# Kernel optimization log

Measured on AMD Instinct MI355X. Metric: run time of the kernel, lower is better.

The kernel has to match this reference:

```python
import jax, jax.numpy as jnp
import numpy as np

NUM_GRAPHS = 64  # number of graphs in the batch (static for segment reductions)


def gcn_conv(x, row, col, ew, W, b, N):
    """PyG GCNConv: x@W, symmetric gcn_norm with self-loops (weight 1), scatter-add, +bias."""
    xw = x @ W  # [N, F_out]
    # degree includes self-loop weight of 1.0 per node
    deg = jnp.zeros((N,), x.dtype).at[col].add(ew) + 1.0
    dis = jnp.where(deg > 0, jax.lax.rsqrt(deg), 0.0)  # deg^{-1/2}, inf -> 0
    norm = dis[row] * ew * dis[col]  # [E]
    agg = jnp.zeros_like(xw).at[col].add(xw[row] * norm[:, None])
    agg = agg + xw * (dis * dis)[:, None]  # self-loop contribution: 1/deg
    return agg + b


def global_mean_pool(x, batch, num_graphs):
    s = jnp.zeros((num_graphs, x.shape[1]), x.dtype).at[batch].add(x)
    cnt = jnp.zeros((num_graphs,), x.dtype).at[batch].add(1.0)
    return s / jnp.maximum(cnt, 1.0)[:, None]


def setup_inputs() -> dict:
    key = jax.random.key(0)
    ks = jax.random.split(key, 10)
    N, E, C_in, C_hid, C_out = 40000, 640000, 128, 128, 64
    flat = 6 * 22 * 22  # num_time_intervals * (2*num_nodes)^2 = 2904
    x = jax.random.normal(ks[0], (N, C_in), jnp.float32)
    edge_index = jax.random.randint(ks[1], (2, E), 0, N, jnp.int64)
    edge_weight = jax.random.uniform(ks[2], (E,), jnp.float32)
    batch = jnp.sort(jax.random.randint(ks[3], (N,), 0, NUM_GRAPHS, jnp.int64))
    W1 = jax.random.normal(ks[4], (C_in, C_hid), jnp.float32) / np.sqrt(C_in)
    b1 = jnp.zeros((C_hid,), jnp.float32)
    W2 = jax.random.normal(ks[5], (C_hid, C_out), jnp.float32) / np.sqrt(C_hid)
    b2 = jnp.zeros((C_out,), jnp.float32)
    Wfc = jax.random.normal(ks[6], (C_out, flat), jnp.float32) / np.sqrt(C_out)
    bfc = jnp.zeros((flat,), jnp.float32)
    return {"x": x, "edge_index": edge_index, "edge_weight": edge_weight, "batch": batch,
            "W1": W1, "b1": b1, "W2": W2, "b2": b2, "Wfc": Wfc, "bfc": bfc}


def reference(x, edge_index, edge_weight, batch, W1, b1, W2, b2, Wfc, bfc):
    N = x.shape[0]
    row, col = edge_index[0], edge_index[1]
    h = jax.nn.relu(gcn_conv(x, row, col, edge_weight, W1, b1, N))
    h = jax.nn.relu(gcn_conv(h, row, col, edge_weight, W2, b2, N))
    g = global_mean_pool(h, batch, NUM_GRAPHS)  # [G, C_out]
    return g @ Wfc + bfc  # [G, 2904] predicted flattened adjacency
```

## Files before the change

### kernel.cpp

```cpp
#include <hip/hip_runtime.h>
#include <hip/hip_bf16.h>
#include <hip/hip_fp16.h>
#include <type_traits>

#define NG 64
#define FLAT 2904
#define K128 128
#define BKB 256

typedef _Float16 h4 __attribute__((ext_vector_type(4)));
typedef _Float16 half8 __attribute__((ext_vector_type(8)));
typedef float f32x4 __attribute__((ext_vector_type(4)));

__device__ __forceinline__ float4 ld4(const float* p) { return *(const float4*)p; }
__device__ __forceinline__ void st4(float* p, float4 v) { *(float4*)p = v; }
__device__ __forceinline__ float4 ldh4(const _Float16* p) {
    h4 h = *(const h4*)p;
    return make_float4((float)h.x, (float)h.y, (float)h.z, (float)h.w);
}
__device__ __forceinline__ void sth4(_Float16* p, float4 v) {
    h4 h; h.x = (_Float16)v.x; h.y = (_Float16)v.y; h.z = (_Float16)v.z; h.w = (_Float16)v.w;
    *(h4*)p = h;
}

__global__ __launch_bounds__(256) void k_zero(int* __restrict__ bhist,
                                              float* __restrict__ g,
                                              int* __restrict__ gcnt) {
    int tid = threadIdx.x;
    for (int i = tid; i < BKB; i += 256) bhist[i] = 0;
    for (int i = tid; i < NG * 64; i += 256) g[i] = 0.f;
    if (tid < NG) gcnt[tid] = 0;
}


__global__ __launch_bounds__(256) void k_bhist(const int* __restrict__ col,
                                               int* __restrict__ bhist, int E, int nbk) {
    __shared__ int h[BKB];
    int tid = threadIdx.x;
    for (int i = tid; i < nbk; i += 256) h[i] = 0;
    __syncthreads();
    int base = blockIdx.x * 1024 + tid * 4;
#pragma unroll
    for (int q = 0; q < 4; q++) {
        int e = base + q;
        if (e < E) atomicAdd(&h[col[e] >> 8], 1);
    }
    __syncthreads();
    for (int i = tid; i < nbk; i += 256) if (h[i]) atomicAdd(&bhist[i], h[i]);
}

__global__ __launch_bounds__(256) void k_bscan(const int* __restrict__ bhist,
                                               int* __restrict__ bbase,
                                               int* __restrict__ bcursor,
                                               int* __restrict__ rsN, int E, int nbk) {
    __shared__ int part[256];
    int tid = threadIdx.x;
    int v = (tid < nbk) ? bhist[tid] : 0;
    part[tid] = v;
    __syncthreads();
    for (int off = 1; off < 256; off <<= 1) {
        int t = (tid >= off) ? part[tid - off] : 0;
        __syncthreads();
        part[tid] += t;
        __syncthreads();
    }
    if (tid < nbk) { int ex = part[tid] - v; bbase[tid] = ex; bcursor[tid] = ex; }
    if (tid == nbk - 1) bbase[nbk] = part[tid];
    if (tid == 0) *rsN = E;
}

__global__ __launch_bounds__(256) void k_bucket(const int* __restrict__ row,
                                                const int* __restrict__ col,
                                                const float* __restrict__ ew,
                                                int* __restrict__ bcursor,
                                                uint2* __restrict__ bk, int E, int nbk) {
    __shared__ int h[BKB];
    __shared__ int cur[BKB];
    int tid = threadIdx.x;
    for (int i = tid; i < nbk; i += 256) h[i] = 0;
    __syncthreads();
    int base = blockIdx.x * 1024 + tid * 4;
    int c[4];
#pragma unroll
    for (int q = 0; q < 4; q++) {
        int e = base + q;
        c[q] = (e < E) ? col[e] : -1;
        if (c[q] >= 0) atomicAdd(&h[c[q] >> 8], 1);
    }
    __syncthreads();
    for (int i = tid; i < nbk; i += 256) cur[i] = h[i] ? atomicAdd(&bcursor[i], h[i]) : 0;
    __syncthreads();
#pragma unroll
    for (int q = 0; q < 4; q++) {
        int e = base + q;
        if (c[q] >= 0) {
            int slot = atomicAdd(&cur[c[q] >> 8], 1);
            bk[slot] = make_uint2(((unsigned)c[q] << 16) | (unsigned)row[e],
                                  __float_as_uint(ew[e]));
        }
    }
}

__global__ __launch_bounds__(256) void k_colsedata(const uint2* __restrict__ bk,
                                                   const int* __restrict__ bbase,
                                                   float* __restrict__ dis,
                                                   int* __restrict__ rs,
                                                   int2* __restrict__ edata, int N) {
    __shared__ float sdeg[BKB];
    __shared__ int scnt[BKB];
    __shared__ int part[BKB];
    __shared__ int cur[BKB];
    __shared__ float sdis[BKB];
    int b = blockIdx.x, tid = threadIdx.x;
    sdeg[tid] = 0.f; scnt[tid] = 0;
    __syncthreads();
    int s = bbase[b], e = bbase[b + 1];
    for (int i = s + tid; i < e; i += 256) {
        uint2 q = bk[i];
        int c8 = (q.x >> 16) & 255;
        atomicAdd(&sdeg[c8], __uint_as_float(q.y));
        atomicAdd(&scnt[c8], 1);
    }
    __syncthreads();
    int cnt = scnt[tid];
    part[tid] = cnt;
    __syncthreads();
    for (int off = 1; off < 256; off <<= 1) {
        int t = (tid >= off) ? part[tid - off] : 0;
        __syncthreads();
        part[tid] += t;
        __syncthreads();
    }
    float d  = rsqrtf(sdeg[tid] + 1.0f);
    int   r0 = s + part[tid] - cnt;
    int gcol = b * BKB + tid;
    if (gcol < N) { dis[gcol] = d; rs[gcol] = r0; }
    cur[tid] = r0; sdis[tid] = d;
    __syncthreads();
    for (int i = s + tid; i < e; i += 256) {
        uint2 q = bk[i];
        int c8 = (q.x >> 16) & 255;
        int r  = q.x & 0xFFFF;
        float w = __uint_as_float(q.y) * sdis[c8];
        int pos = atomicAdd(&cur[c8], 1);
        edata[pos] = make_int2(r, __float_as_int(w));
    }
}

__global__ __launch_bounds__(256) void k_wconv2(const float* __restrict__ W1,
                                                const float* __restrict__ W2,
                                                _Float16* __restrict__ Wt1,
                                                _Float16* __restrict__ Wt2) {
    int idx = blockIdx.x * 256 + threadIdx.x;
    if (idx < 128 * 128) {
        int n = idx % 128, k = idx / 128;
        Wt1[n * K128 + k] = (_Float16)W1[k * 128 + n];
    } else {
        int i = idx - 128 * 128;
        if (i < 64 * 128) {
            int n = i % 64, k = i / 64;
            Wt2[n * K128 + k] = (_Float16)W2[k * 64 + n];
        }
    }
}

template <int NCOL, typename AT>
__global__ __launch_bounds__(256) void k_gemm(const AT* __restrict__ A,
                                              const _Float16* __restrict__ Wt,
                                              const float* __restrict__ dis,
                                              _Float16* __restrict__ out, int M) {
    constexpr int AS = 136;
    __shared__ _Float16 Ah[64 * AS];
    __shared__ _Float16 Wh[NCOL * AS];

    int tid  = threadIdx.x;
    int row0 = blockIdx.x * 64;

    if constexpr (std::is_same_v<AT, float>) {
#pragma unroll
        for (int q = 0; q < 8; q++) {
            int idx = tid + 256 * q;
            int r = idx >> 5, c4 = (idx & 31) * 4;
            float4 v = ld4(A + (size_t)(row0 + r) * K128 + c4);
            sth4(&Ah[r * AS + c4], v);
        }
    } else {
#pragma unroll
        for (int q = 0; q < 4; q++) {
            int idx = tid + 256 * q;
            int r = idx >> 4, c8 = (idx & 15) * 8;
            *(half8*)&Ah[r * AS + c8] = *(const half8*)(A + (size_t)(row0 + r) * K128 + c8);
        }
    }
#pragma unroll
    for (int q = 0; q < NCOL / 16; q++) {
        int idx = tid + 256 * q;
        int n = idx >> 4, c8 = (idx & 15) * 8;
        *(half8*)&Wh[n * AS + c8] = *(const half8*)(Wt + n * K128 + c8);
    }
    __syncthreads();

    int lane = tid & 63;
    int wv   = tid >> 6;
    int m    = lane & 15;
    int quad = lane >> 4;

    f32x4 acc[NCOL / 16];
#pragma unroll
    for (int ct = 0; ct < NCOL / 16; ct++) acc[ct] = (f32x4){0.f, 0.f, 0.f, 0.f};

#pragma unroll
    for (int kt = 0; kt < 4; kt++) {
        half8 af = *(const half8*)&Ah[(wv * 16 + m) * AS + kt * 32 + quad * 8];
#pragma unroll
        for (int ct = 0; ct < NCOL / 16; ct++) {
            half8 bf = *(const half8*)&Wh[(ct * 16 + m) * AS + kt * 32 + quad * 8];
            acc[ct] = __builtin_amdgcn_mfma_f32_16x16x32_f16(af, bf, acc[ct], 0, 0, 0);
        }
    }

    float d[4];
#pragma unroll
    for (int r = 0; r < 4; r++) d[r] = dis[row0 + wv * 16 + quad * 4 + r];
#pragma unroll
    for (int ct = 0; ct < NCOL / 16; ct++) {
#pragma unroll
        for (int r = 0; r < 4; r++) {
            int grow = row0 + wv * 16 + quad * 4 + r;
            out[(size_t)grow * NCOL + ct * 16 + m] = (_Float16)(acc[ct][r] * d[r]);
        }
    }
}

__global__ __launch_bounds__(256) void k_agg128(const _Float16* __restrict__ xw,
                                                const float* __restrict__ dis,
                                                const int2* __restrict__ edata,
                                                const int* __restrict__ rs,
                                                const float* __restrict__ bias,
                                                _Float16* __restrict__ out, int N) {
    constexpr int F = 128;
    int node = blockIdx.x * 8 + (threadIdx.x >> 5);
    int j4   = (threadIdx.x & 31) * 4;
    float dv = dis[node];
    float4 self = ldh4(xw + (size_t)node * F + j4);
    float4 bv   = ld4(bias + j4);
    float4 a0 = make_float4(self.x * dv + bv.x, self.y * dv + bv.y,
                            self.z * dv + bv.z, self.w * dv + bv.w);
    float4 a1 = make_float4(0.f, 0.f, 0.f, 0.f);
    float4 a2 = a1, a3 = a1, a4 = a1, a5 = a1, a6 = a1, a7 = a1;
    int s = rs[node], e = rs[node + 1];
    int j = s;
    for (; j + 8 <= e; j += 8) {
        int2 q0 = edata[j + 0], q1 = edata[j + 1], q2 = edata[j + 2], q3 = edata[j + 3];
        int2 q4 = edata[j + 4], q5 = edata[j + 5], q6 = edata[j + 6], q7 = edata[j + 7];
        float4 v0 = ldh4(xw + (size_t)q0.x * F + j4);
        float4 v1 = ldh4(xw + (size_t)q1.x * F + j4);
        float4 v2 = ldh4(xw + (size_t)q2.x * F + j4);
        float4 v3 = ldh4(xw + (size_t)q3.x * F + j4);
        float4 v4 = ldh4(xw + (size_t)q4.x * F + j4);
        float4 v5 = ldh4(xw + (size_t)q5.x * F + j4);
        float4 v6 = ldh4(xw + (size_t)q6.x * F + j4);
        float4 v7 = ldh4(xw + (size_t)q7.x * F + j4);
        float n0 = __int_as_float(q0.y), n1 = __int_as_float(q1.y);
        float n2 = __int_as_float(q2.y), n3 = __int_as_float(q3.y);
        float n4 = __int_as_float(q4.y), n5 = __int_as_float(q5.y);
        float n6 = __int_as_float(q6.y), n7 = __int_as_float(q7.y);
        a0.x += n0 * v0.x; a0.y += n0 * v0.y; a0.z += n0 * v0.z; a0.w += n0 * v0.w;
        a1.x += n1 * v1.x; a1.y += n1 * v1.y; a1.z += n1 * v1.z; a1.w += n1 * v1.w;
        a2.x += n2 * v2.x; a2.y += n2 * v2.y; a2.z += n2 * v2.z; a2.w += n2 * v2.w;
        a3.x += n3 * v3.x; a3.y += n3 * v3.y; a3.z += n3 * v3.z; a3.w += n3 * v3.w;
        a4.x += n4 * v4.x; a4.y += n4 * v4.y; a4.z += n4 * v4.z; a4.w += n4 * v4.w;
        a5.x += n5 * v5.x; a5.y += n5 * v5.y; a5.z += n5 * v5.z; a5.w += n5 * v5.w;
        a6.x += n6 * v6.x; a6.y += n6 * v6.y; a6.z += n6 * v6.z; a6.w += n6 * v6.w;
        a7.x += n7 * v7.x; a7.y += n7 * v7.y; a7.z += n7 * v7.z; a7.w += n7 * v7.w;
    }
    for (; j + 4 <= e; j += 4) {
        int2 q0 = edata[j + 0], q1 = edata[j + 1], q2 = edata[j + 2], q3 = edata[j + 3];
        float4 v0 = ldh4(xw + (size_t)q0.x * F + j4);
        float4 v1 = ldh4(xw + (size_t)q1.x * F + j4);
        float4 v2 = ldh4(xw + (size_t)q2.x * F + j4);
        float4 v3 = ldh4(xw + (size_t)q3.x * F + j4);
        float n0 = __int_as_float(q0.y), n1 = __int_as_float(q1.y);
        float n2 = __int_as_float(q2.y), n3 = __int_as_float(q3.y);
        a0.x += n0 * v0.x; a0.y += n0 * v0.y; a0.z += n0 * v0.z; a0.w += n0 * v0.w;
        a1.x += n1 * v1.x; a1.y += n1 * v1.y; a1.z += n1 * v1.z; a1.w += n1 * v1.w;
        a2.x += n2 * v2.x; a2.y += n2 * v2.y; a2.z += n2 * v2.z; a2.w += n2 * v2.w;
        a3.x += n3 * v3.x; a3.y += n3 * v3.y; a3.z += n3 * v3.z; a3.w += n3 * v3.w;
    }
    for (; j < e; j++) {
        int2 q = edata[j];
        float nm = __int_as_float(q.y);
        float4 v = ldh4(xw + (size_t)q.x * F + j4);
        a0.x += nm * v.x; a0.y += nm * v.y; a0.z += nm * v.z; a0.w += nm * v.w;
    }
    float4 acc;
    acc.x = ((a0.x + a1.x) + (a2.x + a3.x)) + ((a4.x + a5.x) + (a6.x + a7.x));
    acc.y = ((a0.y + a1.y) + (a2.y + a3.y)) + ((a4.y + a5.y) + (a6.y + a7.y));
    acc.z = ((a0.z + a1.z) + (a2.z + a3.z)) + ((a4.z + a5.z) + (a6.z + a7.z));
    acc.w = ((a0.w + a1.w) + (a2.w + a3.w)) + ((a4.w + a5.w) + (a6.w + a7.w));
    acc.x = fmaxf(acc.x, 0.f); acc.y = fmaxf(acc.y, 0.f);
    acc.z = fmaxf(acc.z, 0.f); acc.w = fmaxf(acc.w, 0.f);
    sth4(out + (size_t)node * F + j4, acc);
}

__global__ __launch_bounds__(256) void k_agg_pool(const _Float16* __restrict__ xw,
                                                  const float* __restrict__ dis,
                                                  const int2* __restrict__ edata,
                                                  const int* __restrict__ rs,
                                                  const float* __restrict__ bias,
                                                  const int* __restrict__ batch,
                                                  float* __restrict__ g,
                                                  int* __restrict__ gcnt, int N) {
    constexpr int F = 64;
    __shared__ float T[16][F + 4];
    __shared__ int sb[16];
    int tid  = threadIdx.x;
    int base = blockIdx.x * 16;
    int nl   = tid >> 4;
    int node = base + nl;
    int j4   = (tid & 15) * 4;
    if (tid < 16) sb[tid] = batch[base + tid];

    float dv = dis[node];
    float4 self = ldh4(xw + (size_t)node * F + j4);
    float4 bv   = ld4(bias + j4);
    float4 a0 = make_float4(self.x * dv + bv.x, self.y * dv + bv.y,
                            self.z * dv + bv.z, self.w * dv + bv.w);
    float4 a1 = make_float4(0.f, 0.f, 0.f, 0.f);
    float4 a2 = a1, a3 = a1;
    int s = rs[node], e = rs[node + 1];
    int j = s;
    for (; j + 4 <= e; j += 4) {
        int2 q0 = edata[j + 0], q1 = edata[j + 1], q2 = edata[j + 2], q3 = edata[j + 3];
        float4 v0 = ldh4(xw + (size_t)q0.x * F + j4);
        float4 v1 = ldh4(xw + (size_t)q1.x * F + j4);
        float4 v2 = ldh4(xw + (size_t)q2.x * F + j4);
        float4 v3 = ldh4(xw + (size_t)q3.x * F + j4);
        float n0 = __int_as_float(q0.y), n1 = __int_as_float(q1.y);
        float n2 = __int_as_float(q2.y), n3 = __int_as_float(q3.y);
        a0.x += n0 * v0.x; a0.y += n0 * v0.y; a0.z += n0 * v0.z; a0.w += n0 * v0.w;
        a1.x += n1 * v1.x; a1.y += n1 * v1.y; a1.z += n1 * v1.z; a1.w += n1 * v1.w;
        a2.x += n2 * v2.x; a2.y += n2 * v2.y; a2.z += n2 * v2.z; a2.w += n2 * v2.w;
        a3.x += n3 * v3.x; a3.y += n3 * v3.y; a3.z += n3 * v3.z; a3.w += n3 * v3.w;
    }
    for (; j < e; j++) {
        int2 q = edata[j];
        float nm = __int_as_float(q.y);
        float4 v = ldh4(xw + (size_t)q.x * F + j4);
        a0.x += nm * v.x; a0.y += nm * v.y; a0.z += nm * v.z; a0.w += nm * v.w;
    }
    float4 acc;
    acc.x = (a0.x + a1.x) + (a2.x + a3.x);
    acc.y = (a0.y + a1.y) + (a2.y + a3.y);
    acc.z = (a0.z + a1.z) + (a2.z + a3.z);
    acc.w = (a0.w + a1.w) + (a2.w + a3.w);
    T[nl][j4 + 0] = fmaxf(acc.x, 0.f);
    T[nl][j4 + 1] = fmaxf(acc.y, 0.f);
    T[nl][j4 + 2] = fmaxf(acc.z, 0.f);
    T[nl][j4 + 3] = fmaxf(acc.w, 0.f);
    __syncthreads();
    if (tid < 64) {
        int f = tid;
        float run = 0.f;
        int cur = -1, cnt = 0;
        for (int k = 0; k < 16; k++) {
            int b = sb[k];
            if (b != cur) {
                if (cur >= 0) {
                    atomicAdd(&g[cur * 64 + f], run);
                    if (f == 0) atomicAdd(&gcnt[cur], cnt);
                }
                cur = b; run = 0.f; cnt = 0;
            }
            run += T[k][f];
            cnt++;
        }
        atomicAdd(&g[cur * 64 + f], run);
        if (f == 0) atomicAdd(&gcnt[cur], cnt);
    }
}

__global__ __launch_bounds__(256) void k_fc(const float* __restrict__ g,
                                            const int* __restrict__ gcnt,
                                            const float* __restrict__ Wfc,
                                            const float* __restrict__ bfc,
                                            float* __restrict__ out) {
    __shared__ float gs[64];
    int i = blockIdx.y;
    int j = blockIdx.x * blockDim.x + threadIdx.x;
    if (threadIdx.x < 64) {
        float c = (float)gcnt[i];
        gs[threadIdx.x] = g[i * 64 + threadIdx.x] / fmaxf(c, 1.0f);
    }
    __syncthreads();
    if (j >= FLAT) return;
    float acc = bfc[j];
#pragma unroll 8
    for (int k = 0; k < 64; k++) acc += gs[k] * Wfc[k * FLAT + j];
    out[(size_t)i * FLAT + j] = acc;
}

extern "C" void kernel_launch(void* const* d_in, const int* in_sizes, int n_in,
                              void* d_out, int out_size, void* d_ws, size_t ws_size,
                              hipStream_t stream) {
    const float* x    = (const float*)d_in[0];
    const int*   ei   = (const int*)d_in[1];
    const float* ew   = (const float*)d_in[2];
    const int*   batch= (const int*)d_in[3];
    const float* W1   = (const float*)d_in[4];
    const float* b1   = (const float*)d_in[5];
    const float* W2   = (const float*)d_in[6];
    const float* b2   = (const float*)d_in[7];
    const float* Wfc  = (const float*)d_in[8];
    const float* bfc  = (const float*)d_in[9];
    float* out = (float*)d_out;

    const int N = in_sizes[0] / K128;
    const int E = in_sizes[2];
    const int* row = ei;
    const int* col = ei + E;
    const int nbk = (N + BKB - 1) / BKB;
    const int neb = (E + 1023) / 1024;

    char* p = (char*)d_ws;
    auto alloc = [&](size_t bytes) -> void* {
        void* r = (void*)p;
        p += (bytes + 255) & ~(size_t)255;
        return r;
    };
    float*     dis   = (float*)    alloc((size_t)N * 4);
    int*       rs    = (int*)      alloc((size_t)(N + 1) * 4);
    uint2*     bk    = (uint2*)    alloc((size_t)E * 8);
    int2*      edata = (int2*)     alloc((size_t)E * 8);
    _Float16*  xw1   = (_Float16*) alloc((size_t)N * 128 * 2);
    _Float16*  h1    = (_Float16*) alloc((size_t)N * 128 * 2);
    _Float16*  xw2   = (_Float16*) alloc((size_t)N * 64 * 2);
    _Float16*  Wt1   = (_Float16*) alloc((size_t)128 * 128 * 2);
    _Float16*  Wt2   = (_Float16*) alloc((size_t)64 * 128 * 2);
    float*     g     = (float*)    alloc(64 * 64 * 4);
    int*       gcnt  = (int*)      alloc(64 * 4);
    int*       bhist = (int*)      alloc(BKB * 4);
    int*       bbase = (int*)      alloc((BKB + 2) * 4);
    int*       bcur  = (int*)      alloc(BKB * 4);

    k_zero     <<<1,   256, 0, stream>>>(bhist, g, gcnt);
    k_bhist    <<<neb, 256, 0, stream>>>(col, bhist, E, nbk);
    k_bscan    <<<1,   256, 0, stream>>>(bhist, bbase, bcur, rs + N, E, nbk);
    k_bucket   <<<neb, 256, 0, stream>>>(row, col, ew, bcur, bk, E, nbk);
    k_colsedata<<<nbk, 256, 0, stream>>>(bk, bbase, dis, rs, edata, N);
    k_wconv2   <<<(192 * 128 + 255) / 256, 256, 0, stream>>>(W1, W2, Wt1, Wt2);

    k_gemm<128, float><<<N / 64, 256, 0, stream>>>(x, Wt1, dis, xw1, N);
    k_agg128<<<N / 8, 256, 0, stream>>>(xw1, dis, edata, rs, b1, h1, N);

    k_gemm<64, _Float16><<<N / 64, 256, 0, stream>>>(h1, Wt2, dis, xw2, N);
    k_agg_pool<<<N / 16, 256, 0, stream>>>(xw2, dis, edata, rs, b2, batch, g, gcnt, N);

    dim3 fcg((FLAT + 255) / 256, NG);
    k_fc<<<fcg, 256, 0, stream>>>(g, gcnt, Wfc, bfc, out);
}
```

Measured before the change: 203.6 us.

## Fuse layer-1 aggregation with layer-2 GEMM, pack edges, drop scan and conversion kernels

Fuses the first-layer neighbour aggregation with the second-layer GEMM, so h1 is kept in shared memory and no longer written to and reread from global memory. Edge records are packed into 32 bits (16-bit row index plus fp16 weight), halving edge-stream traffic in both aggregation passes. The bucket prefix scan is recomputed redundantly inside each consumer block instead of in a separate kernel, and weight conversion is merged into the init kernel, which removes several launches. The risks are fp16 precision loss on the edge norms and extra per-block scan work.

```diff
diff --git a/kernel.cpp b/kernel.cpp
--- a/kernel.cpp
+++ b/kernel.cpp
@@ -13,7 +13,6 @@
 typedef float f32x4 __attribute__((ext_vector_type(4)));
 
 __device__ __forceinline__ float4 ld4(const float* p) { return *(const float4*)p; }
-__device__ __forceinline__ void st4(float* p, float4 v) { *(float4*)p = v; }
 __device__ __forceinline__ float4 ldh4(const _Float16* p) {
     h4 h = *(const h4*)p;
     return make_float4((float)h.x, (float)h.y, (float)h.z, (float)h.w);
@@ -22,14 +21,33 @@
     h4 h; h.x = (_Float16)v.x; h.y = (_Float16)v.y; h.z = (_Float16)v.z; h.w = (_Float16)v.w;
     *(h4*)p = h;
 }
-
-__global__ __launch_bounds__(256) void k_zero(int* __restrict__ bhist,
+__device__ __forceinline__ float unpack_w(unsigned q) {
+    return (float)__builtin_bit_cast(_Float16, (unsigned short)(q & 0xFFFFu));
+}
+
+__global__ __launch_bounds__(256) void k_init(int* __restrict__ bhist,
+                                              int* __restrict__ bcursor,
                                               float* __restrict__ g,
-                                              int* __restrict__ gcnt) {
+                                              int* __restrict__ gcnt,
+                                              const float* __restrict__ W1,
+                                              const float* __restrict__ W2,
+                                              _Float16* __restrict__ Wt1,
+                                              _Float16* __restrict__ Wt2) {
     int tid = threadIdx.x;
-    for (int i = tid; i < BKB; i += 256) bhist[i] = 0;
-    for (int i = tid; i < NG * 64; i += 256) g[i] = 0.f;
-    if (tid < NG) gcnt[tid] = 0;
+    if (blockIdx.x == 0) {
+        bhist[tid] = 0; bcursor[tid] = 0;
+        for (int i = tid; i < NG * 64; i += 256) g[i] = 0.f;
+        if (tid < NG) gcnt[tid] = 0;
+    }
+    int idx = blockIdx.x * 256 + tid;
+    if (idx < 128 * 128) {
+        int n = idx % 128, k = idx / 128;
+        Wt1[n * K128 + k] = (_Float16)W1[k * 128 + n];
+    } else if (idx < 128 * 128 + 64 * 128) {
+        int i = idx - 128 * 128;
+        int n = i % 64, k = i / 64;
+        Wt2[n * K128 + k] = (_Float16)W2[k * 64 + n];
+    }
 }
 
 
@@ -49,36 +67,27 @@
     for (int i = tid; i < nbk; i += 256) if (h[i]) atomicAdd(&bhist[i], h[i]);
 }
 
-__global__ __launch_bounds__(256) void k_bscan(const int* __restrict__ bhist,
-                                               int* __restrict__ bbase,
-                                               int* __restrict__ bcursor,
-                                               int* __restrict__ rsN, int E, int nbk) {
-    __shared__ int part[256];
-    int tid = threadIdx.x;
-    int v = (tid < nbk) ? bhist[tid] : 0;
-    part[tid] = v;
-    __syncthreads();
-    for (int off = 1; off < 256; off <<= 1) {
-        int t = (tid >= off) ? part[tid - off] : 0;
-        __syncthreads();
-        part[tid] += t;
-        __syncthreads();
-    }
-    if (tid < nbk) { int ex = part[tid] - v; bbase[tid] = ex; bcursor[tid] = ex; }
-    if (tid == nbk - 1) bbase[nbk] = part[tid];
-    if (tid == 0) *rsN = E;
-}
-
 __global__ __launch_bounds__(256) void k_bucket(const int* __restrict__ row,
                                                 const int* __restrict__ col,
                                                 const float* __restrict__ ew,
+                                                const int* __restrict__ bhist,
                                                 int* __restrict__ bcursor,
                                                 uint2* __restrict__ bk, int E, int nbk) {
+    __shared__ int part[256];
     __shared__ int h[BKB];
     __shared__ int cur[BKB];
     int tid = threadIdx.x;
-    for (int i = tid; i < nbk; i += 256) h[i] = 0;
-    __syncthreads();
+    int gh = (tid < nbk) ? bhist[tid] : 0;
+    part[tid] = gh;
+    h[tid] = 0;
+    __syncthreads();
+    for (int off = 1; off < 256; off <<= 1) {
+        int t = (tid >= off) ? part[tid - off] : 0;
+        __syncthreads();
+        part[tid] += t;
+        __syncthreads();
+    }
+    int ex = part[tid] - gh;
     int base = blockIdx.x * 1024 + tid * 4;
     int c[4];
 #pragma unroll
@@ -88,7 +97,7 @@
         if (c[q] >= 0) atomicAdd(&h[c[q] >> 8], 1);
     }
     __syncthreads();
-    for (int i = tid; i < nbk; i += 256) cur[i] = h[i] ? atomicAdd(&bcursor[i], h[i]) : 0;
+    if (tid < nbk) cur[tid] = h[tid] ? ex + atomicAdd(&bcursor[tid], h[tid]) : 0;
     __syncthreads();
 #pragma unroll
     for (int q = 0; q < 4; q++) {
@@ -102,19 +111,31 @@
 }
 
 __global__ __launch_bounds__(256) void k_colsedata(const uint2* __restrict__ bk,
-                                                   const int* __restrict__ bbase,
+                                                   const int* __restrict__ bhist,
                                                    float* __restrict__ dis,
                                                    int* __restrict__ rs,
-                                                   int2* __restrict__ edata, int N) {
+                                                   unsigned* __restrict__ edata,
+                                                   int N, int E, int nbk) {
+    __shared__ int part[256];
     __shared__ float sdeg[BKB];
     __shared__ int scnt[BKB];
-    __shared__ int part[BKB];
     __shared__ int cur[BKB];
     __shared__ float sdis[BKB];
+    __shared__ int sse[2];
     int b = blockIdx.x, tid = threadIdx.x;
+    int gh = (tid < nbk) ? bhist[tid] : 0;
+    part[tid] = gh;
     sdeg[tid] = 0.f; scnt[tid] = 0;
     __syncthreads();
-    int s = bbase[b], e = bbase[b + 1];
+    for (int off = 1; off < 256; off <<= 1) {
+        int t = (tid >= off) ? part[tid - off] : 0;
+        __syncthreads();
+        part[tid] += t;
+        __syncthreads();
+    }
+    if (tid == b) { sse[0] = part[tid] - gh; sse[1] = part[tid]; }
+    __syncthreads();
+    int s = sse[0], e = sse[1];
     for (int i = s + tid; i < e; i += 256) {
         uint2 q = bk[i];
         int c8 = (q.x >> 16) & 255;
@@ -135,62 +156,35 @@
     int   r0 = s + part[tid] - cnt;
     int gcol = b * BKB + tid;
     if (gcol < N) { dis[gcol] = d; rs[gcol] = r0; }
+    if (b == 0 && tid == 0) rs[N] = E;
     cur[tid] = r0; sdis[tid] = d;
     __syncthreads();
     for (int i = s + tid; i < e; i += 256) {
         uint2 q = bk[i];
         int c8 = (q.x >> 16) & 255;
-        int r  = q.x & 0xFFFF;
-        float w = __uint_as_float(q.y) * sdis[c8];
+        unsigned r = q.x & 0xFFFFu;
+        _Float16 wh = (_Float16)(__uint_as_float(q.y) * sdis[c8]);
         int pos = atomicAdd(&cur[c8], 1);
-        edata[pos] = make_int2(r, __float_as_int(w));
-    }
-}
-
-__global__ __launch_bounds__(256) void k_wconv2(const float* __restrict__ W1,
-                                                const float* __restrict__ W2,
-                                                _Float16* __restrict__ Wt1,
-                                                _Float16* __restrict__ Wt2) {
-    int idx = blockIdx.x * 256 + threadIdx.x;
-    if (idx < 128 * 128) {
-        int n = idx % 128, k = idx / 128;
-        Wt1[n * K128 + k] = (_Float16)W1[k * 128 + n];
-    } else {
-        int i = idx - 128 * 128;
-        if (i < 64 * 128) {
-            int n = i % 64, k = i / 64;
-            Wt2[n * K128 + k] = (_Float16)W2[k * 64 + n];
-        }
-    }
-}
-
-template <int NCOL, typename AT>
-__global__ __launch_bounds__(256) void k_gemm(const AT* __restrict__ A,
-                                              const _Float16* __restrict__ Wt,
-                                              const float* __restrict__ dis,
-                                              _Float16* __restrict__ out, int M) {
-    constexpr int AS = 136;
+        edata[pos] = (r << 16) | (unsigned)__builtin_bit_cast(unsigned short, wh);
+    }
+}
+
+__global__ __launch_bounds__(256) void k_gemm1(const float* __restrict__ A,
+                                               const _Float16* __restrict__ Wt,
+                                               const float* __restrict__ dis,
+                                               _Float16* __restrict__ out, int M) {
+    constexpr int NCOL = 128, AS = 136;
     __shared__ _Float16 Ah[64 * AS];
     __shared__ _Float16 Wh[NCOL * AS];
 
     int tid  = threadIdx.x;
     int row0 = blockIdx.x * 64;
-
-    if constexpr (std::is_same_v<AT, float>) {
-#pragma unroll
-        for (int q = 0; q < 8; q++) {
-            int idx = tid + 256 * q;
-            int r = idx >> 5, c4 = (idx & 31) * 4;
-            float4 v = ld4(A + (size_t)(row0 + r) * K128 + c4);
-            sth4(&Ah[r * AS + c4], v);
-        }
-    } else {
-#pragma unroll
-        for (int q = 0; q < 4; q++) {
-            int idx = tid + 256 * q;
-            int r = idx >> 4, c8 = (idx & 15) * 8;
-            *(half8*)&Ah[r * AS + c8] = *(const half8*)(A + (size_t)(row0 + r) * K128 + c8);
-        }
+#pragma unroll
+    for (int q = 0; q < 8; q++) {
+        int idx = tid + 256 * q;
+        int r = idx >> 5, c4 = (idx & 31) * 4;
+        float4 v = ld4(A + (size_t)(row0 + r) * K128 + c4);
+        sth4(&Ah[r * AS + c4], v);
     }
 #pragma unroll
     for (int q = 0; q < NCOL / 16; q++) {
@@ -200,15 +194,10 @@
     }
     __syncthreads();
 
-    int lane = tid & 63;
-    int wv   = tid >> 6;
-    int m    = lane & 15;
-    int quad = lane >> 4;
-
+    int lane = tid & 63, wv = tid >> 6, m = lane & 15, quad = lane >> 4;
     f32x4 acc[NCOL / 16];
 #pragma unroll
     for (int ct = 0; ct < NCOL / 16; ct++) acc[ct] = (f32x4){0.f, 0.f, 0.f, 0.f};
-
 #pragma unroll
     for (int kt = 0; kt < 4; kt++) {
         half8 af = *(const half8*)&Ah[(wv * 16 + m) * AS + kt * 32 + quad * 8];
@@ -218,94 +207,102 @@
             acc[ct] = __builtin_amdgcn_mfma_f32_16x16x32_f16(af, bf, acc[ct], 0, 0, 0);
         }
     }
-
     float d[4];
 #pragma unroll
     for (int r = 0; r < 4; r++) d[r] = dis[row0 + wv * 16 + quad * 4 + r];
 #pragma unroll
-    for (int ct = 0; ct < NCOL / 16; ct++) {
+    for (int ct = 0; ct < NCOL / 16; ct++)
 #pragma unroll
         for (int r = 0; r < 4; r++) {
             int grow = row0 + wv * 16 + quad * 4 + r;
             out[(size_t)grow * NCOL + ct * 16 + m] = (_Float16)(acc[ct][r] * d[r]);
         }
-    }
-}
-
-__global__ __launch_bounds__(256) void k_agg128(const _Float16* __restrict__ xw,
-                                                const float* __restrict__ dis,
-                                                const int2* __restrict__ edata,
-                                                const int* __restrict__ rs,
-                                                const float* __restrict__ bias,
-                                                _Float16* __restrict__ out, int N) {
-    constexpr int F = 128;
-    int node = blockIdx.x * 8 + (threadIdx.x >> 5);
-    int j4   = (threadIdx.x & 31) * 4;
-    float dv = dis[node];
-    float4 self = ldh4(xw + (size_t)node * F + j4);
-    float4 bv   = ld4(bias + j4);
-    float4 a0 = make_float4(self.x * dv + bv.x, self.y * dv + bv.y,
-                            self.z * dv + bv.z, self.w * dv + bv.w);
-    float4 a1 = make_float4(0.f, 0.f, 0.f, 0.f);
-    float4 a2 = a1, a3 = a1, a4 = a1, a5 = a1, a6 = a1, a7 = a1;
+}
+
+__global__ __launch_bounds__(256) void k_agg_gemm(const _Float16* __restrict__ xw,
+                                                  const float* __restrict__ dis,
+                                                  const unsigned* __restrict__ edata,
+                                                  const int* __restrict__ rs,
+                                                  const float* __restrict__ bias,
+                                                  const _Float16* __restrict__ Wt2,
+                                                  _Float16* __restrict__ xw2, int N) {
+    constexpr int F = 128, AS = 136;
+    __shared__ _Float16 Hs[16 * AS];
+    __shared__ _Float16 Ws[64 * AS];
+
+    int tid   = threadIdx.x;
+    int node0 = blockIdx.x * 16;
+    int nl    = tid >> 4;
+    int node  = node0 + nl;
+    int j8    = (tid & 15) * 8;
+
+#pragma unroll
+    for (int q = 0; q < 4; q++) {
+        int idx = tid + 256 * q;
+        int n = idx >> 4, c8 = (idx & 15) * 8;
+        *(half8*)&Ws[n * AS + c8] = *(const half8*)(Wt2 + n * K128 + c8);
+    }
+
+    float a0[8], a1[8], a2[8], a3[8];
+    {
+        float dv = dis[node];
+        half8 sv = *(const half8*)(xw + (size_t)node * F + j8);
+        float4 bA = ld4(bias + j8), bB = ld4(bias + j8 + 4);
+#pragma unroll
+        for (int t = 0; t < 4; t++) { a0[t] = (float)sv[t] * dv + (&bA.x)[t];
+                                      a0[t + 4] = (float)sv[t + 4] * dv + (&bB.x)[t]; }
+#pragma unroll
+        for (int t = 0; t < 8; t++) { a1[t] = 0.f; a2[t] = 0.f; a3[t] = 0.f; }
+    }
     int s = rs[node], e = rs[node + 1];
     int j = s;
-    for (; j + 8 <= e; j += 8) {
-        int2 q0 = edata[j + 0], q1 = edata[j + 1], q2 = edata[j + 2], q3 = edata[j + 3];
-        int2 q4 = edata[j + 4], q5 = edata[j + 5], q6 = edata[j + 6], q7 = edata[j + 7];
-        float4 v0 = ldh4(xw + (size_t)q0.x * F + j4);
-        float4 v1 = ldh4(xw + (size_t)q1.x * F + j4);
-        float4 v2 = ldh4(xw + (size_t)q2.x * F + j4);
-        float4 v3 = ldh4(xw + (size_t)q3.x * F + j4);
-        float4 v4 = ldh4(xw + (size_t)q4.x * F + j4);
-        float4 v5 = ldh4(xw + (size_t)q5.x * F + j4);
-        float4 v6 = ldh4(xw + (size_t)q6.x * F + j4);
-        float4 v7 = ldh4(xw + (size_t)q7.x * F + j4);
-        float n0 = __int_as_float(q0.y), n1 = __int_as_float(q1.y);
-        float n2 = __int_as_float(q2.y), n3 = __int_as_float(q3.y);
-        float n4 = __int_as_float(q4.y), n5 = __int_as_float(q5.y);
-        float n6 = __int_as_float(q6.y), n7 = __int_as_float(q7.y);
-        a0.x += n0 * v0.x; a0.y += n0 * v0.y; a0.z += n0 * v0.z; a0.w += n0 * v0.w;
-        a1.x += n1 * v1.x; a1.y += n1 * v1.y; a1.z += n1 * v1.z; a1.w += n1 * v1.w;
-        a2.x += n2 * v2.x; a2.y += n2 * v2.y; a2.z += n2 * v2.z; a2.w += n2 * v2.w;
-        a3.x += n3 * v3.x; a3.y += n3 * v3.y; a3.z += n3 * v3.z; a3.w += n3 * v3.w;
-        a4.x += n4 * v4.x; a4.y += n4 * v4.y; a4.z += n4 * v4.z; a4.w += n4 * v4.w;
-        a5.x += n5 * v5.x; a5.y += n5 * v5.y; a5.z += n5 * v5.z; a5.w += n5 * v5.w;
-        a6.x += n6 * v6.x; a6.y += n6 * v6.y; a6.z += n6 * v6.z; a6.w += n6 * v6.w;
-        a7.x += n7 * v7.x; a7.y += n7 * v7.y; a7.z += n7 * v7.z; a7.w += n7 * v7.w;
-    }
     for (; j + 4 <= e; j += 4) {
-        int2 q0 = edata[j + 0], q1 = edata[j + 1], q2 = edata[j + 2], q3 = edata[j + 3];
-        float4 v0 = ldh4(xw + (size_t)q0.x * F + j4);
-        float4 v1 = ldh4(xw + (size_t)q1.x * F + j4);
-        float4 v2 = ldh4(xw + (size_t)q2.x * F + j4);
-        float4 v3 = ldh4(xw + (size_t)q3.x * F + j4);
-        float n0 = __int_as_float(q0.y), n1 = __int_as_float(q1.y);
-        float n2 = __int_as_float(q2.y), n3 = __int_as_float(q3.y);
-        a0.x += n0 * v0.x; a0.y += n0 * v0.y; a0.z += n0 * v0.z; a0.w += n0 * v0.w;
-        a1.x += n1 * v1.x; a1.y += n1 * v1.y; a1.z += n1 * v1.z; a1.w += n1 * v1.w;
-        a2.x += n2 * v2.x; a2.y += n2 * v2.y; a2.z += n2 * v2.z; a2.w += n2 * v2.w;
-        a3.x += n3 * v3.x; a3.y += n3 * v3.y; a3.z += n3 * v3.z; a3.w += n3 * v3.w;
+        unsigned q0 = edata[j + 0], q1 = edata[j + 1], q2 = edata[j + 2], q3 = edata[j + 3];
+        half8 v0 = *(const half8*)(xw + (size_t)(q0 >> 16) * F + j8);
+        half8 v1 = *(const half8*)(xw + (size_t)(q1 >> 16) * F + j8);
+        half8 v2 = *(const half8*)(xw + (size_t)(q2 >> 16) * F + j8);
+        half8 v3 = *(const half8*)(xw + (size_t)(q3 >> 16) * F + j8);
+        float n0 = unpack_w(q0), n1 = unpack_w(q1), n2 = unpack_w(q2), n3 = unpack_w(q3);
+#pragma unroll
+        for (int t = 0; t < 8; t++) {
+            a0[t] += n0 * (float)v0[t];
+            a1[t] += n1 * (float)v1[t];
+            a2[t] += n2 * (float)v2[t];
+            a3[t] += n3 * (float)v3[t];
+        }
     }
     for (; j < e; j++) {
-        int2 q = edata[j];
-        float nm = __int_as_float(q.y);
-        float4 v = ldh4(xw + (size_t)q.x * F + j4);
-        a0.x += nm * v.x; a0.y += nm * v.y; a0.z += nm * v.z; a0.w += nm * v.w;
-    }
-    float4 acc;
-    acc.x = ((a0.x + a1.x) + (a2.x + a3.x)) + ((a4.x + a5.x) + (a6.x + a7.x));
-    acc.y = ((a0.y + a1.y) + (a2.y + a3.y)) + ((a4.y + a5.y) + (a6.y + a7.y));
-    acc.z = ((a0.z + a1.z) + (a2.z + a3.z)) + ((a4.z + a5.z) + (a6.z + a7.z));
-    acc.w = ((a0.w + a1.w) + (a2.w + a3.w)) + ((a4.w + a5.w) + (a6.w + a7.w));
-    acc.x = fmaxf(acc.x, 0.f); acc.y = fmaxf(acc.y, 0.f);
-    acc.z = fmaxf(acc.z, 0.f); acc.w = fmaxf(acc.w, 0.f);
-    sth4(out + (size_t)node * F + j4, acc);
+        unsigned q = edata[j];
+        half8 v = *(const half8*)(xw + (size_t)(q >> 16) * F + j8);
+        float nm = unpack_w(q);
+#pragma unroll
+        for (int t = 0; t < 8; t++) a0[t] += nm * (float)v[t];
+    }
+    half8 hv;
+#pragma unroll
+    for (int t = 0; t < 8; t++)
+        hv[t] = (_Float16)fmaxf((a0[t] + a1[t]) + (a2[t] + a3[t]), 0.f);
+    *(half8*)&Hs[nl * AS + j8] = hv;
+    __syncthreads();
+
+    int lane = tid & 63, wv = tid >> 6, m = lane & 15, quad = lane >> 4;
+    f32x4 acc = (f32x4){0.f, 0.f, 0.f, 0.f};
+#pragma unroll
+    for (int kt = 0; kt < 4; kt++) {
+        half8 af = *(const half8*)&Hs[m * AS + kt * 32 + quad * 8];
+        half8 bf = *(const half8*)&Ws[(wv * 16 + m) * AS + kt * 32 + quad * 8];
+        acc = __builtin_amdgcn_mfma_f32_16x16x32_f16(af, bf, acc, 0, 0, 0);
+    }
+#pragma unroll
+    for (int r = 0; r < 4; r++) {
+        int gn = node0 + quad * 4 + r;
+        xw2[(size_t)gn * 64 + wv * 16 + m] = (_Float16)(acc[r] * dis[gn]);
+    }
 }
 
 __global__ __launch_bounds__(256) void k_agg_pool(const _Float16* __restrict__ xw,
                                                   const float* __restrict__ dis,
-                                                  const int2* __restrict__ edata,
+                                                  const unsigned* __restrict__ edata,
                                                   const int* __restrict__ rs,
                                                   const float* __restrict__ bias,
                                                   const int* __restrict__ batch,
@@ -331,33 +328,27 @@
     int s = rs[node], e = rs[node + 1];
     int j = s;
     for (; j + 4 <= e; j += 4) {
-        int2 q0 = edata[j + 0], q1 = edata[j + 1], q2 = edata[j + 2], q3 = edata[j + 3];
-        float4 v0 = ldh4(xw + (size_t)q0.x * F + j4);
-        float4 v1 = ldh4(xw + (size_t)q1.x * F + j4);
-        float4 v2 = ldh4(xw + (size_t)q2.x * F + j4);
-        float4 v3 = ldh4(xw + (size_t)q3.x * F + j4);
-        float n0 = __int_as_float(q0.y), n1 = __int_as_float(q1.y);
-        float n2 = __int_as_float(q2.y), n3 = __int_as_float(q3.y);
+        unsigned q0 = edata[j + 0], q1 = edata[j + 1], q2 = edata[j + 2], q3 = edata[j + 3];
+        float4 v0 = ldh4(xw + (size_t)(q0 >> 16) * F + j4);
+        float4 v1 = ldh4(xw + (size_t)(q1 >> 16) * F + j4);
+        float4 v2 = ldh4(xw + (size_t)(q2 >> 16) * F + j4);
+        float4 v3 = ldh4(xw + (size_t)(q3 >> 16) * F + j4);
+        float n0 = unpack_w(q0), n1 = unpack_w(q1), n2 = unpack_w(q2), n3 = unpack_w(q3);
         a0.x += n0 * v0.x; a0.y += n0 * v0.y; a0.z += n0 * v0.z; a0.w += n0 * v0.w;
         a1.x += n1 * v1.x; a1.y += n1 * v1.y; a1.z += n1 * v1.z; a1.w += n1 * v1.w;
         a2.x += n2 * v2.x; a2.y += n2 * v2.y; a2.z += n2 * v2.z; a2.w += n2 * v2.w;
         a3.x += n3 * v3.x; a3.y += n3 * v3.y; a3.z += n3 * v3.z; a3.w += n3 * v3.w;
     }
     for (; j < e; j++) {
-        int2 q = edata[j];
-        float nm = __int_as_float(q.y);
-        float4 v = ldh4(xw + (size_t)q.x * F + j4);
+        unsigned q = edata[j];
+        float nm = unpack_w(q);
+        float4 v = ldh4(xw + (size_t)(q >> 16) * F + j4);
         a0.x += nm * v.x; a0.y += nm * v.y; a0.z += nm * v.z; a0.w += nm * v.w;
     }
-    float4 acc;
-    acc.x = (a0.x + a1.x) + (a2.x + a3.x);
-    acc.y = (a0.y + a1.y) + (a2.y + a3.y);
-    acc.z = (a0.z + a1.z) + (a2.z + a3.z);
-    acc.w = (a0.w + a1.w) + (a2.w + a3.w);
-    T[nl][j4 + 0] = fmaxf(acc.x, 0.f);
-    T[nl][j4 + 1] = fmaxf(acc.y, 0.f);
-    T[nl][j4 + 2] = fmaxf(acc.z, 0.f);
-    T[nl][j4 + 3] = fmaxf(acc.w, 0.f);
+    T[nl][j4 + 0] = fmaxf((a0.x + a1.x) + (a2.x + a3.x), 0.f);
+    T[nl][j4 + 1] = fmaxf((a0.y + a1.y) + (a2.y + a3.y), 0.f);
+    T[nl][j4 + 2] = fmaxf((a0.z + a1.z) + (a2.z + a3.z), 0.f);
+    T[nl][j4 + 3] = fmaxf((a0.w + a1.w) + (a2.w + a3.w), 0.f);
     __syncthreads();
     if (tid < 64) {
         int f = tid;
@@ -431,30 +422,24 @@
     float*     dis   = (float*)    alloc((size_t)N * 4);
     int*       rs    = (int*)      alloc((size_t)(N + 1) * 4);
     uint2*     bk    = (uint2*)    alloc((size_t)E * 8);
-    int2*      edata = (int2*)     alloc((size_t)E * 8);
+    unsigned*  edata = (unsigned*) alloc((size_t)E * 4);
     _Float16*  xw1   = (_Float16*) alloc((size_t)N * 128 * 2);
-    _Float16*  h1    = (_Float16*) alloc((size_t)N * 128 * 2);
     _Float16*  xw2   = (_Float16*) alloc((size_t)N * 64 * 2);
     _Float16*  Wt1   = (_Float16*) alloc((size_t)128 * 128 * 2);
     _Float16*  Wt2   = (_Float16*) alloc((size_t)64 * 128 * 2);
     float*     g     = (float*)    alloc(64 * 64 * 4);
     int*       gcnt  = (int*)      alloc(64 * 4);
     int*       bhist = (int*)      alloc(BKB * 4);
-    int*       bbase = (int*)      alloc((BKB + 2) * 4);
     int*       bcur  = (int*)      alloc(BKB * 4);
 
-    k_zero     <<<1,   256, 0, stream>>>(bhist, g, gcnt);
+    k_init     <<<96,  256, 0, stream>>>(bhist, bcur, g, gcnt, W1, W2, Wt1, Wt2);
     k_bhist    <<<neb, 256, 0, stream>>>(col, bhist, E, nbk);
-    k_bscan    <<<1,   256, 0, stream>>>(bhist, bbase, bcur, rs + N, E, nbk);
-    k_bucket   <<<neb, 256, 0, stream>>>(row, col, ew, bcur, bk, E, nbk);
-    k_colsedata<<<nbk, 256, 0, stream>>>(bk, bbase, dis, rs, edata, N);
-    k_wconv2   <<<(192 * 128 + 255) / 256, 256, 0, stream>>>(W1, W2, Wt1, Wt2);
-
-    k_gemm<128, float><<<N / 64, 256, 0, stream>>>(x, Wt1, dis, xw1, N);
-    k_agg128<<<N / 8, 256, 0, stream>>>(xw1, dis, edata, rs, b1, h1, N);
-
-    k_gemm<64, _Float16><<<N / 64, 256, 0, stream>>>(h1, Wt2, dis, xw2, N);
-    k_agg_pool<<<N / 16, 256, 0, stream>>>(xw2, dis, edata, rs, b2, batch, g, gcnt, N);
+    k_bucket   <<<neb, 256, 0, stream>>>(row, col, ew, bhist, bcur, bk, E, nbk);
+    k_colsedata<<<nbk, 256, 0, stream>>>(bk, bhist, dis, rs, edata, N, E, nbk);
+
+    k_gemm1    <<<N / 64, 256, 0, stream>>>(x, Wt1, dis, xw1, N);
+    k_agg_gemm <<<N / 16, 256, 0, stream>>>(xw1, dis, edata, rs, b1, Wt2, xw2, N);
+    k_agg_pool <<<N / 16, 256, 0, stream>>>(xw2, dis, edata, rs, b2, batch, g, gcnt, N);
 
     dim3 fcg((FLAT + 255) / 256, NG);
     k_fc<<<fcg, 256, 0, stream>>>(g, gcnt, Wfc, bfc, out);
```

Measured after the change: 195.0 us, median of 2. 1.04x faster.
